# Optimization experiments

Hardware: AMD Instinct MI355X
Metric: run time of the kernel (lower is better)

## Reference

```python
import jax, jax.numpy as jnp
import numpy as np

B, S, E = 2, 2048, 4096
HQ, HKV, D = 32, 8, 128
WINDOW = 1024
SOFT_CAP = 50.0
Q_PRE_ATTN = 128.0
TT_SCALE = 0.1
TT_FLOOR = 8192.0
EPS = 1e-6
ROPE_BASE = 10000.0


def l2norm(x):
    return x * jax.lax.rsqrt(jnp.mean(x * x, axis=-1, keepdims=True) + EPS)


def apply_rope(x, pos):
    # x: [B,S,H,D]; half-split rotary, base 10000
    half = x.shape[-1] // 2
    freq = ROPE_BASE ** (-jnp.arange(half, dtype=jnp.float32) * 2.0 / x.shape[-1])  # [half]
    angle = pos.astype(jnp.float32)[:, None] * freq[None, :]                         # [S,half]
    cos = jnp.cos(angle)[None, :, None, :]
    sin = jnp.sin(angle)[None, :, None, :]
    x1, x2 = x[..., :half], x[..., half:]
    return jnp.concatenate([x1 * cos - x2 * sin, x2 * cos + x1 * sin], axis=-1)


def setup_inputs() -> dict:
    key = jax.random.key(0)
    ks = jax.random.split(key, 5)
    sc = 0.02
    return {
        "x": jax.random.normal(ks[0], (B, S, E), jnp.float32),
        "Wq": jax.random.normal(ks[1], (E, HQ, D), jnp.float32) * sc,
        "Wk": jax.random.normal(ks[2], (E, HKV, D), jnp.float32) * sc,
        "Wv": jax.random.normal(ks[3], (E, HKV, D), jnp.float32) * sc,
        "Wo": jax.random.normal(ks[4], (HQ, D, E), jnp.float32) * sc,
    }


def reference(x, Wq, Wk, Wv, Wo):
    pos = jnp.arange(S)
    # QKV projections
    q = jnp.einsum('bse,ehd->bshd', x, Wq)   # [B,S,HQ,D]
    k = jnp.einsum('bse,ehd->bshd', x, Wk)   # [B,S,HKV,D]
    v = jnp.einsum('bse,ehd->bshd', x, Wv)   # [B,S,HKV,D]
    # QK norm (L2Norm) then RoPE
    q = apply_rope(l2norm(q), pos)
    k = apply_rope(l2norm(k), pos)
    # query pre-attention scaling
    q = q * (Q_PRE_ATTN ** -0.5)
    # temperature tuning: per-position scale
    attn_scale = jnp.log(jnp.floor((pos.astype(jnp.float32) + 1.0) / TT_FLOOR) + 1.0) * TT_SCALE + 1.0
    q = q * attn_scale[None, :, None, None]
    # GQA: expand kv heads
    g = HQ // HKV
    k_r = jnp.repeat(k, g, axis=2)           # [B,S,HQ,D]
    v_r = jnp.repeat(v, g, axis=2)
    logits = jnp.einsum('bihd,bjhd->bhij', q, k_r).astype(jnp.float32)
    # tanh soft cap
    logits = SOFT_CAP * jnp.tanh(logits / SOFT_CAP)
    # causal + sliding window mask: j <= i and i - j < WINDOW
    i = pos[:, None]
    j = pos[None, :]
    mask = (j <= i) & ((i - j) < WINDOW)     # [S,S]
    logits = jnp.where(mask[None, None], logits, jnp.float32(-1e30))
    probs = jax.nn.softmax(logits, axis=-1)
    out = jnp.einsum('bhij,bjhd->bihd', probs, v_r)  # [B,S,HQ,D]
    return jnp.einsum('bihd,hde->bie', out, Wo)      # [B,S,E]
```

## Files before the change

kernel.cpp:

```cpp
#include <hip/hip_runtime.h>


typedef unsigned short u16;
typedef unsigned int   u32;
typedef __bf16 bf16x8 __attribute__((ext_vector_type(8)));
typedef float  f32x4  __attribute__((ext_vector_type(4)));

typedef __attribute__((address_space(1))) void* gas_ptr;
typedef __attribute__((address_space(3))) void* las_ptr;

__device__ __forceinline__ void load_lds16(const void* g, void* l) {
  __builtin_amdgcn_global_load_lds((gas_ptr)g, (las_ptr)l, 16, 0, 0);
}

__device__ __forceinline__ u16 f2bf(float f) {
  u32 u = __builtin_bit_cast(u32, f);
  u += 0x7fffu + ((u >> 16) & 1u);
  return (u16)(u >> 16);
}
__device__ __forceinline__ float bf2f(u16 h) {
  u32 u = ((u32)h) << 16;
  return __builtin_bit_cast(float, u);
}
__device__ __forceinline__ u32 pack_trunc(float a, float b) {
  return (__builtin_bit_cast(u32, a) >> 16) | (__builtin_bit_cast(u32, b) & 0xffff0000u);
}

__global__ __launch_bounds__(256) void cast_f32_bf16(const float* __restrict__ src,
                                                     u16* __restrict__ dst) {
  size_t i = ((size_t)blockIdx.x * 256 + threadIdx.x) * 8;
  float4 a = *(const float4*)(src + i);
  float4 b = *(const float4*)(src + i + 4);
  uint4 o;
  o.x = (u32)f2bf(a.x) | ((u32)f2bf(a.y) << 16);
  o.y = (u32)f2bf(a.z) | ((u32)f2bf(a.w) << 16);
  o.z = (u32)f2bf(b.x) | ((u32)f2bf(b.y) << 16);
  o.w = (u32)f2bf(b.z) | ((u32)f2bf(b.w) << 16);
  *(uint4*)(dst + i) = o;
}

__global__ __launch_bounds__(256) void transpose_cast_f32_bf16(
    const float* __restrict__ src, u16* __restrict__ dst, int R, int C) {
  __shared__ float tile[32][33];
  const int tx = threadIdx.x & 31, ty = threadIdx.x >> 5;
  const int r0 = blockIdx.y * 32, c0 = blockIdx.x * 32;
#pragma unroll
  for (int i = 0; i < 4; ++i)
    tile[ty + i * 8][tx] = src[(size_t)(r0 + ty + i * 8) * C + (c0 + tx)];
  __syncthreads();
#pragma unroll
  for (int i = 0; i < 4; ++i)
    dst[(size_t)(c0 + ty + i * 8) * R + (r0 + tx)] = f2bf(tile[tx][ty + i * 8]);
}

__global__ __launch_bounds__(256) void transpose_v(const u16* __restrict__ src,
                                                   u16* __restrict__ dst) {
  __shared__ u16 tile[32][34];
  const int plane = blockIdx.z;
  const u16* s = src + (size_t)plane * 2048 * 128;
  u16* d = dst + (size_t)plane * 2048 * 128;
  const int tx = threadIdx.x & 31, ty = threadIdx.x >> 5;
  const int r0 = blockIdx.x * 32, c0 = blockIdx.y * 32;
#pragma unroll
  for (int i = 0; i < 4; ++i)
    tile[ty + i * 8][tx] = s[(size_t)(r0 + ty + i * 8) * 128 + (c0 + tx)];
  __syncthreads();
#pragma unroll
  for (int i = 0; i < 4; ++i)
    d[(size_t)(c0 + ty + i * 8) * 2048 + (r0 + tx)] = tile[tx][ty + i * 8];
}


template <int MB>
__device__ __forceinline__ void mm16(f32x4 (&acc)[8][4], const bf16x8 (&af)[4],
                                     const bf16x8 (&bf)[4]) {
#pragma unroll
  for (int ii = 0; ii < 4; ++ii)
#pragma unroll
    for (int nf = 0; nf < 4; ++nf)
      acc[MB + ii][nf] =
          __builtin_amdgcn_mfma_f32_16x16x32_bf16(af[ii], bf[nf], acc[MB + ii][nf], 0, 0, 0);
}

template <int OUT_BF16>
__global__ __launch_bounds__(512, 2) void gemm256(const u16* __restrict__ A,
                                                  const u16* __restrict__ Bt,
                                                  void* __restrict__ Cout,
                                                  int N, int K, int ntx) {
  __shared__ __align__(16) u16 lds[65536];
  const int t = threadIdx.x, lane = t & 63, w = t >> 6;
  const int c = lane & 15, q = lane >> 4;
  const int wm = w >> 2, wn = w & 3;

  const int cpx = (int)gridDim.x >> 3;
  const int swz = ((int)blockIdx.x & 7) * cpx + ((int)blockIdx.x >> 3);
  const int bx = swz % ntx, by = swz / ntx;
  const int m0 = by << 8, n0 = bx << 8;

  u32 aoff[2][2], boff[2][2];
#pragma unroll
  for (int h = 0; h < 2; ++h)
#pragma unroll
    for (int j = 0; j < 2; ++j) {
      const int rowS = w * 16 + j * 8 + (lane >> 3);
      const int colE = ((lane & 7) ^ (rowS & 7)) * 8;
      aoff[h][j] = (u32)(m0 + h * 128 + rowS) * (u32)K + (u32)colE;
      boff[h][j] = (u32)(n0 + h * 128 + rowS) * (u32)K + (u32)colE;
    }
  const u32 stW = (u32)w * 1024u;

  const u32 sl0 = (u32)((q ^ (c & 7)) * 8);
  const u32 aR = (u32)(wm * 8192 + c * 64) + sl0;
  const u32 bR = (u32)(16384 + (wn >> 1) * 8192 + (wn & 1) * 4096 + c * 64) + sl0;

  f32x4 acc[8][4];
#pragma unroll
  for (int i2 = 0; i2 < 8; ++i2)
#pragma unroll
    for (int j2 = 0; j2 < 4; ++j2) acc[i2][j2] = (f32x4){0.f, 0.f, 0.f, 0.f};

  const int nt = K >> 6;

#define STG_A(bb, hh, kt)                                                \
  do {                                                                   \
    u16* d_ = &lds[(bb) * 32768u + (hh) * 8192u + stW];                  \
    load_lds16(A + (aoff[hh][0] + (u32)(kt) * 64u), d_);                 \
    load_lds16(A + (aoff[hh][1] + (u32)(kt) * 64u), d_ + 512);           \
  } while (0)
#define STG_B(bb, hh, kt)                                                \
  do {                                                                   \
    u16* d_ = &lds[(bb) * 32768u + 16384u + (hh) * 8192u + stW];         \
    load_lds16(Bt + (boff[hh][0] + (u32)(kt) * 64u), d_);                \
    load_lds16(Bt + (boff[hh][1] + (u32)(kt) * 64u), d_ + 512);          \
  } while (0)
#define RD4(dst, base)                                                   \
  do {                                                                   \
    const u16* p_ = &lds[(base)];                                        \
    dst[0] = *(const bf16x8*)(p_);                                       \
    dst[1] = *(const bf16x8*)(p_ + 1024);                                \
    dst[2] = *(const bf16x8*)(p_ + 2048);                                \
    dst[3] = *(const bf16x8*)(p_ + 3072);                                \
  } while (0)
#define BAR __builtin_amdgcn_s_barrier()
#define LGKM0 asm volatile("s_waitcnt lgkmcnt(0)" ::: "memory")
#define LGKM8 asm volatile("s_waitcnt lgkmcnt(8)" ::: "memory")
#define VM6 asm volatile("s_waitcnt vmcnt(6)" ::: "memory")
#define PRIO1 __builtin_amdgcn_s_setprio(1)
#define PRIO0 __builtin_amdgcn_s_setprio(0)

  STG_B(0, 0, 0);
  STG_B(0, 1, 0);
  STG_A(0, 0, 0);
  STG_A(0, 1, 0);
  STG_B(1, 0, 1);
  STG_B(1, 1, 1);
  STG_A(1, 0, 1);
  VM6;
  BAR;

  bf16x8 Bf0[4], Bf1[4], Af0[4], Af1[4];

  for (int i = 0; i < (nt >> 1); ++i) {
    const int tb = 2 * i + 1;
    int t2 = 2 * i + 2; if (t2 >= nt) t2 -= nt;
    int t3 = 2 * i + 3; if (t3 >= nt) t3 -= nt;

    RD4(Bf0, bR);
    RD4(Bf1, bR ^ 32u);
    RD4(Af0, aR);
    STG_A(1, 1, tb);
    LGKM8;
    BAR; LGKM0;
    PRIO1; mm16<0>(acc, Af0, Bf0); PRIO0;
    BAR;
    RD4(Af1, aR + 4096u);
    STG_B(0, 0, t2);
    BAR; LGKM0;
    PRIO1; mm16<4>(acc, Af1, Bf0); PRIO0;
    BAR;
    RD4(Af0, aR ^ 32u);
    RD4(Af1, (aR + 4096u) ^ 32u);
    STG_B(0, 1, t2);
    BAR; LGKM0;
    PRIO1; mm16<0>(acc, Af0, Bf1); PRIO0;
    BAR;
    STG_A(0, 0, t2);
    VM6;
    BAR;
    PRIO1; mm16<4>(acc, Af1, Bf1); PRIO0;
    BAR;

    RD4(Bf0, 32768u + bR);
    RD4(Bf1, (32768u + bR) ^ 32u);
    RD4(Af0, 32768u + aR);
    STG_A(0, 1, t2);
    LGKM8;
    BAR; LGKM0;
    PRIO1; mm16<0>(acc, Af0, Bf0); PRIO0;
    BAR;
    RD4(Af1, 32768u + aR + 4096u);
    STG_B(1, 0, t3);
    BAR; LGKM0;
    PRIO1; mm16<4>(acc, Af1, Bf0); PRIO0;
    BAR;
    RD4(Af0, (32768u + aR) ^ 32u);
    RD4(Af1, (32768u + aR + 4096u) ^ 32u);
    STG_B(1, 1, t3);
    BAR; LGKM0;
    PRIO1; mm16<0>(acc, Af0, Bf1); PRIO0;
    BAR;
    STG_A(1, 0, t3);
    VM6;
    BAR;
    PRIO1; mm16<4>(acc, Af1, Bf1); PRIO0;
    BAR;
  }

  asm volatile("s_waitcnt vmcnt(0)" ::: "memory");

#undef STG_A
#undef STG_B
#undef RD4
#undef BAR
#undef LGKM0
#undef LGKM8
#undef VM6
#undef PRIO1
#undef PRIO0

  const int rb0 = m0 + wm * 128 + q * 4;
  const int cb0 = n0 + wn * 64 + c;
#pragma unroll
  for (int mf = 0; mf < 8; ++mf)
#pragma unroll
    for (int nf = 0; nf < 4; ++nf) {
      const size_t base = (size_t)(rb0 + mf * 16) * N + (cb0 + nf * 16);
#pragma unroll
      for (int r = 0; r < 4; ++r) {
        if (OUT_BF16)
          ((u16*)Cout)[base + (size_t)r * N] = f2bf(acc[mf][nf][r]);
        else
          ((float*)Cout)[base + (size_t)r * N] = acc[mf][nf][r];
      }
    }
}

__global__ __launch_bounds__(256) void qkv_post(const u16* __restrict__ raw,
                                                u16* __restrict__ qb,
                                                u16* __restrict__ kb,
                                                u16* __restrict__ vb) {
  const int t = threadIdx.x, lane = t & 63, w = t >> 6;
  const int idx = blockIdx.x * 4 + w;
  const int row = idx / 48, hh = idx - row * 48;
  const int b = row >> 11, pos = row & 2047;
  const u16* base = raw + (size_t)row * 6144 + hh * 128;
  const u16 r1 = base[lane], r2 = base[lane + 64];

  if (hh >= 40) {
    u16* dst = vb + ((size_t)((b * 8 + (hh - 40)) * 2048 + pos)) * 128;
    dst[lane] = r1;
    dst[lane + 64] = r2;
    return;
  }
  float v1 = bf2f(r1), v2 = bf2f(r2);
  float ss = v1 * v1 + v2 * v2;
#pragma unroll
  for (int off = 32; off >= 1; off >>= 1) ss += __shfl_xor(ss, off);
  const float rn = rsqrtf(ss * (1.0f / 128.0f) + 1e-6f);
  const float n1 = v1 * rn, n2 = v2 * rn;
  const float fr = exp2f(-(float)lane * 0.20762050593046f);
  const float ang = (float)pos * fr;
  float sn, cs;
  sincosf(ang, &sn, &cs);
  float o1 = n1 * cs - n2 * sn;
  float o2 = n2 * cs + n1 * sn;
  u16* dst;
  if (hh < 32) {
    const float as_ = logf(floorf((float)(pos + 1) * (1.0f / 8192.0f)) + 1.0f) * 0.1f + 1.0f;
    const float sc = 0.088388347648318447f * as_;
    o1 *= sc;
    o2 *= sc;
    dst = qb + ((size_t)((b * 32 + hh) * 2048 + pos)) * 128;
  } else {
    dst = kb + ((size_t)((b * 8 + (hh - 32)) * 2048 + pos)) * 128;
  }
  dst[lane] = f2bf(o1);
  dst[lane + 64] = f2bf(o2);
}

__global__ __launch_bounds__(256, 4) void attn_fwd(const u16* __restrict__ qb,
                                                   const u16* __restrict__ kb,
                                                   const u16* __restrict__ vtb,
                                                   u16* __restrict__ attn) {
  __shared__ __align__(16) u16 Ks[2][64 * 128];
  __shared__ __align__(16) u16 VTs[2][128 * 64];
  __shared__ __align__(16) u16 Ps[4][16 * 64];

  const int t = threadIdx.x, lane = t & 63, w = t >> 6;
  const int c = lane & 15, quad = lane >> 4;
  const int q0 = blockIdx.x * 64;
  const int bh = blockIdx.y;
  const int b = bh >> 5, hq = bh & 31;
  const int kvp = b * 8 + (hq >> 2);
  const u16* qp = qb + (size_t)bh * (2048 * 128);
  const u16* kp = kb + (size_t)kvp * (2048 * 128);
  const u16* vp = vtb + (size_t)kvp * (128 * 2048);
  u16* Psw = &Ps[w][0];

  bf16x8 qf[4];
  {
    const u16* qrow = qp + (size_t)(q0 + w * 16 + c) * 128 + quad * 8;
#pragma unroll
    for (int ks = 0; ks < 4; ++ks) qf[ks] = *(const bf16x8*)(qrow + ks * 32);
  }

  f32x4 oacc[8];
#pragma unroll
  for (int j = 0; j < 8; ++j)
#pragma unroll
    for (int r = 0; r < 4; ++r) oacc[j][r] = 0.0f;
  float lsum = 0.0f;

  const int i_glob = q0 + w * 16 + c;

  int t0 = q0 - 1023;
  if (t0 < 0) t0 = 0;
  t0 = (t0 >> 6) << 6;

#define STAGE_KV(nb, kvbase)                                                   \
  do {                                                                         \
    const int row_in_ = lane >> 4, ch_ = lane & 15;                            \
    _Pragma("unroll")                                                          \
    for (int i_ = 0; i_ < 4; ++i_) {                                           \
      const int row_ = w * 4 + i_ * 16 + row_in_;                              \
      const int g_ = ch_ ^ (row_ & 15);                                        \
      load_lds16(kp + (size_t)((kvbase) + row_) * 128 + g_ * 8,                \
                 &Ks[nb][(w * 4 + i_ * 16) * 128]);                            \
    }                                                                          \
    const int drow_ = lane >> 3, ch8_ = lane & 7;                              \
    _Pragma("unroll")                                                          \
    for (int i_ = 0; i_ < 4; ++i_) {                                           \
      const int dd_ = w * 8 + i_ * 32 + drow_;                                 \
      const int g_ = ch8_ ^ (dd_ & 7);                                         \
      load_lds16(vp + (size_t)dd_ * 2048 + (kvbase) + g_ * 8,                  \
                 &VTs[nb][(w * 8 + i_ * 32) * 64]);                            \
    }                                                                          \
  } while (0)

  STAGE_KV(0, t0);
  __syncthreads();

  int cur = 0;
  for (int kv0 = t0; kv0 <= q0; kv0 += 64) {
    if (kv0 + 64 <= q0) STAGE_KV(cur ^ 1, kv0 + 64);

    const u16* Kc = &Ks[cur][0];
    const u16* Vc = &VTs[cur][0];

    f32x4 sacc[4];
#pragma unroll
    for (int im = 0; im < 4; ++im)
#pragma unroll
      for (int r = 0; r < 4; ++r) sacc[im][r] = 0.0f;

#pragma unroll
    for (int ks = 0; ks < 4; ++ks) {
#pragma unroll
      for (int im = 0; im < 4; ++im) {
        const int key = im * 16 + c;
        const int ch = (ks * 4 + quad) ^ c;
        const bf16x8 af = *(const bf16x8*)&Kc[key * 128 + ch * 8];
        sacc[im] = __builtin_amdgcn_mfma_f32_16x16x32_bf16(af, qf[ks], sacc[im], 0, 0, 0);
      }
    }

    const bool need_mask = (kv0 == q0) || (q0 - kv0 >= 961);
#pragma unroll
    for (int im = 0; im < 4; ++im) {
      float pv[4];
#pragma unroll
      for (int r = 0; r < 4; ++r) {
        const float s = sacc[im][r];
        const float u = s * s;
        const float cap = s * (1.0f + u * (-1.3333333e-4f + u * 2.1333333e-8f));
        pv[r] = __expf(cap);
      }
      if (need_mask) {
        const int j_base = kv0 + im * 16 + quad * 4;
#pragma unroll
        for (int r = 0; r < 4; ++r) {
          const int j_glob = j_base + r;
          if (!((j_glob <= i_glob) && (i_glob - j_glob < 1024))) pv[r] = 0.0f;
        }
      }
      lsum += (pv[0] + pv[1]) + (pv[2] + pv[3]);
      uint2 pk;
      pk.x = pack_trunc(pv[0], pv[1]);
      pk.y = pack_trunc(pv[2], pv[3]);
      *(uint2*)&Psw[c * 64 + ((im * 2 + (quad >> 1)) ^ (c & 7)) * 8 + (quad & 1) * 4] = pk;
    }

#pragma unroll
    for (int ks = 0; ks < 2; ++ks) {
      const bf16x8 pf = *(const bf16x8*)&Psw[c * 64 + ((ks * 4 + quad) ^ (c & 7)) * 8];
#pragma unroll
      for (int jn = 0; jn < 8; ++jn) {
        const int dd = jn * 16 + c;
        const int ch = (ks * 4 + quad) ^ (c & 7);
        const bf16x8 vf = *(const bf16x8*)&Vc[dd * 64 + ch * 8];
        oacc[jn] = __builtin_amdgcn_mfma_f32_16x16x32_bf16(pf, vf, oacc[jn], 0, 0, 0);
      }
    }

    __syncthreads();
    cur ^= 1;
  }
#undef STAGE_KV

  float lt = lsum;
  lt += __shfl_xor(lt, 16);
  lt += __shfl_xor(lt, 32);
  float rl[4];
#pragma unroll
  for (int r = 0; r < 4; ++r)
    rl[r] = __builtin_amdgcn_rcpf(__shfl(lt, quad * 4 + r));

  const size_t obase = ((size_t)(b * 2048 + q0 + w * 16)) * 4096 + hq * 128;
#pragma unroll
  for (int jn = 0; jn < 8; ++jn) {
#pragma unroll
    for (int r = 0; r < 4; ++r) {
      const int q_in = quad * 4 + r;
      attn[obase + (size_t)q_in * 4096 + jn * 16 + c] = f2bf(oacc[jn][r] * rl[r]);
    }
  }
}

extern "C" void kernel_launch(void* const* d_in, const int* in_sizes, int n_in,
                              void* d_out, int out_size, void* d_ws, size_t ws_size,
                              hipStream_t stream) {
  (void)in_sizes; (void)n_in; (void)out_size; (void)ws_size;
  const float* x  = (const float*)d_in[0];
  const float* Wq = (const float*)d_in[1];
  const float* Wk = (const float*)d_in[2];
  const float* Wv = (const float*)d_in[3];
  const float* Wo = (const float*)d_in[4];
  float* out = (float*)d_out;
  char* ws = (char*)d_ws;

  u16* xb    = (u16*)(ws + 0);
  u16* vtb   = (u16*)(ws + 0);
  u16* WqkvT = (u16*)(ws + 33554432ULL);
  u16* qb    = (u16*)(ws + 33554432ULL);
  u16* kb    = (u16*)(ws + 67108864ULL);
  u16* vb    = (u16*)(ws + 75497472ULL);
  u16* WoT   = (u16*)(ws + 83886080ULL);
  u16* qkvr  = (u16*)(ws + 117440512ULL);
  u16* attnb = (u16*)(ws + 117440512ULL);

  cast_f32_bf16<<<8192, 256, 0, stream>>>(x, xb);
  transpose_cast_f32_bf16<<<dim3(128, 128), 256, 0, stream>>>(Wq, WqkvT, 4096, 4096);
  transpose_cast_f32_bf16<<<dim3(32, 128), 256, 0, stream>>>(Wk, WqkvT + (size_t)4096 * 4096, 4096, 1024);
  transpose_cast_f32_bf16<<<dim3(32, 128), 256, 0, stream>>>(Wv, WqkvT + (size_t)5120 * 4096, 4096, 1024);
  transpose_cast_f32_bf16<<<dim3(128, 128), 256, 0, stream>>>(Wo, WoT, 4096, 4096);

  gemm256<1><<<dim3(384), 512, 0, stream>>>(xb, WqkvT, (void*)qkvr, 6144, 4096, 24);
  qkv_post<<<49152, 256, 0, stream>>>(qkvr, qb, kb, vb);
  transpose_v<<<dim3(64, 4, 16), 256, 0, stream>>>(vb, vtb);
  attn_fwd<<<dim3(32, 64), 256, 0, stream>>>(qb, kb, vtb, attnb);
  gemm256<0><<<dim3(256), 512, 0, stream>>>(attnb, WoT, (void*)out, 4096, 4096, 16);
}
```

Baseline: 725.2 us.

## Halve KV tile to 32 keys, trim causal overrun, and reorder query blocks

```diff
diff --git a/kernel.cpp b/kernel.cpp
--- a/kernel.cpp
+++ b/kernel.cpp
@@ -292,13 +292,15 @@
                                                    const u16* __restrict__ kb,
                                                    const u16* __restrict__ vtb,
                                                    u16* __restrict__ attn) {
-  __shared__ __align__(16) u16 Ks[2][64 * 128];
-  __shared__ __align__(16) u16 VTs[2][128 * 64];
-  __shared__ __align__(16) u16 Ps[4][16 * 64];
+  __shared__ __align__(16) u16 Ks[2][32 * 128];
+  __shared__ __align__(16) u16 VTs[2][128 * 32];
+  __shared__ __align__(16) u16 Ps[4][16 * 32];
 
   const int t = threadIdx.x, lane = t & 63, w = t >> 6;
   const int c = lane & 15, quad = lane >> 4;
-  const int q0 = blockIdx.x * 64;
+  const int swzc = (c & 3) ^ ((c >> 2) & 3);
+  const int bxr = (int)blockIdx.x;
+  const int q0 = ((bxr & 7) * 4 + (bxr >> 3)) * 64;
   const int bh = blockIdx.y;
   const int b = bh >> 5, hq = bh & 31;
   const int kvp = b * 8 + (hq >> 2);
@@ -325,25 +327,24 @@
 
   int t0 = q0 - 1023;
   if (t0 < 0) t0 = 0;
-  t0 = (t0 >> 6) << 6;
+  t0 = (t0 >> 5) << 5;
+  const int last = q0 + 32;
 
 #define STAGE_KV(nb, kvbase)                                                   \
   do {                                                                         \
-    const int row_in_ = lane >> 4, ch_ = lane & 15;                            \
     _Pragma("unroll")                                                          \
-    for (int i_ = 0; i_ < 4; ++i_) {                                           \
-      const int row_ = w * 4 + i_ * 16 + row_in_;                              \
-      const int g_ = ch_ ^ (row_ & 15);                                        \
+    for (int i_ = 0; i_ < 2; ++i_) {                                           \
+      const int row_ = w * 4 + i_ * 16 + (lane >> 4);                          \
+      const int g_ = (lane & 15) ^ (row_ & 15);                                \
       load_lds16(kp + (size_t)((kvbase) + row_) * 128 + g_ * 8,                \
                  &Ks[nb][(w * 4 + i_ * 16) * 128]);                            \
     }                                                                          \
-    const int drow_ = lane >> 3, ch8_ = lane & 7;                              \
+    const int gv_ = (lane & 3) ^ ((lane >> 2) & 3) ^ ((lane >> 4) & 3);        \
     _Pragma("unroll")                                                          \
-    for (int i_ = 0; i_ < 4; ++i_) {                                           \
-      const int dd_ = w * 8 + i_ * 32 + drow_;                                 \
-      const int g_ = ch8_ ^ (dd_ & 7);                                         \
-      load_lds16(vp + (size_t)dd_ * 2048 + (kvbase) + g_ * 8,                  \
-                 &VTs[nb][(w * 8 + i_ * 32) * 64]);                            \
+    for (int i_ = 0; i_ < 2; ++i_) {                                           \
+      const int dd_ = w * 16 + i_ * 64 + (lane >> 2);                          \
+      load_lds16(vp + (size_t)dd_ * 2048 + (kvbase) + gv_ * 8,                 \
+                 &VTs[nb][(w * 16 + i_ * 64) * 32]);                           \
     }                                                                          \
   } while (0)
 
@@ -351,22 +352,22 @@
   __syncthreads();
 
   int cur = 0;
-  for (int kv0 = t0; kv0 <= q0; kv0 += 64) {
-    if (kv0 + 64 <= q0) STAGE_KV(cur ^ 1, kv0 + 64);
+  for (int kv0 = t0; kv0 <= last; kv0 += 32) {
+    if (kv0 + 32 <= last) STAGE_KV(cur ^ 1, kv0 + 32);
 
     const u16* Kc = &Ks[cur][0];
     const u16* Vc = &VTs[cur][0];
 
-    f32x4 sacc[4];
-#pragma unroll
-    for (int im = 0; im < 4; ++im)
+    f32x4 sacc[2];
+#pragma unroll
+    for (int im = 0; im < 2; ++im)
 #pragma unroll
       for (int r = 0; r < 4; ++r) sacc[im][r] = 0.0f;
 
 #pragma unroll
     for (int ks = 0; ks < 4; ++ks) {
 #pragma unroll
-      for (int im = 0; im < 4; ++im) {
+      for (int im = 0; im < 2; ++im) {
         const int key = im * 16 + c;
         const int ch = (ks * 4 + quad) ^ c;
         const bf16x8 af = *(const bf16x8*)&Kc[key * 128 + ch * 8];
@@ -374,9 +375,9 @@
       }
     }
 
-    const bool need_mask = (kv0 == q0) || (q0 - kv0 >= 961);
-#pragma unroll
-    for (int im = 0; im < 4; ++im) {
+    const bool need_mask = (kv0 > q0 - 32) || (kv0 <= q0 - 961);
+#pragma unroll
+    for (int im = 0; im < 2; ++im) {
       float pv[4];
 #pragma unroll
       for (int r = 0; r < 4; ++r) {
@@ -397,17 +398,15 @@
       uint2 pk;
       pk.x = pack_trunc(pv[0], pv[1]);
       pk.y = pack_trunc(pv[2], pv[3]);
-      *(uint2*)&Psw[c * 64 + ((im * 2 + (quad >> 1)) ^ (c & 7)) * 8 + (quad & 1) * 4] = pk;
-    }
-
-#pragma unroll
-    for (int ks = 0; ks < 2; ++ks) {
-      const bf16x8 pf = *(const bf16x8*)&Psw[c * 64 + ((ks * 4 + quad) ^ (c & 7)) * 8];
+      *(uint2*)&Psw[c * 32 + (((im * 2 + (quad >> 1)) ^ swzc)) * 8 + (quad & 1) * 4] = pk;
+    }
+
+    {
+      const bf16x8 pf = *(const bf16x8*)&Psw[c * 32 + ((quad ^ swzc)) * 8];
 #pragma unroll
       for (int jn = 0; jn < 8; ++jn) {
         const int dd = jn * 16 + c;
-        const int ch = (ks * 4 + quad) ^ (c & 7);
-        const bf16x8 vf = *(const bf16x8*)&Vc[dd * 64 + ch * 8];
+        const bf16x8 vf = *(const bf16x8*)&Vc[dd * 32 + ((quad ^ swzc)) * 8];
         oacc[jn] = __builtin_amdgcn_mfma_f32_16x16x32_bf16(pf, vf, oacc[jn], 0, 0, 0);
       }
     }
```

Result: no change. 722.4 us (-0.4%).
